# Kernel tuning notes

Measured on AMD Instinct MI355X. Metric: run time of the kernel, lower is better.

The kernel has to match this reference:

```python
import jax, jax.numpy as jnp
import numpy as np

N_NODES = 50000


def _gin_layer(feat, src, dst, W, b):
    # sum-aggregate neighbor (src) features onto dst nodes, eps=0
    agg = jax.ops.segment_sum(feat[src], dst, num_segments=N_NODES)
    return (feat + agg) @ W + b


def setup_inputs() -> dict:
    key = jax.random.key(0)
    ks = jax.random.split(key, 8)
    n, e, d, c = N_NODES, 1600000, 128, 4
    feat = jax.random.normal(ks[0], (n, d), dtype=jnp.float32)
    src = jax.random.randint(ks[1], (e,), 0, n, dtype=jnp.int64)
    dst = jax.random.randint(ks[2], (e,), 0, n, dtype=jnp.int64)
    s = 1.0 / np.sqrt(d)
    W0 = jax.random.normal(ks[3], (d, d), dtype=jnp.float32) * s
    W1 = jax.random.normal(ks[4], (d, d), dtype=jnp.float32) * s
    W2 = jax.random.normal(ks[5], (d, d), dtype=jnp.float32) * s
    W3 = jax.random.normal(ks[6], (d, c), dtype=jnp.float32) * s
    return {
        "feat": feat, "src": src, "dst": dst,
        "W0": W0, "b0": jnp.zeros((d,), jnp.float32),
        "W1": W1, "b1": jnp.zeros((d,), jnp.float32),
        "W2": W2, "b2": jnp.zeros((d,), jnp.float32),
        "W3": W3, "b3": jnp.zeros((c,), jnp.float32),
    }


def reference(feat, src, dst, W0, b0, W1, b1, W2, b2, W3, b3):
    # 3 hidden GINConv layers with ReLU (dropout p=0 / eval -> identity)
    h = jax.nn.relu(_gin_layer(feat, src, dst, W0, b0))
    h = jax.nn.relu(_gin_layer(h, src, dst, W1, b1))
    h = jax.nn.relu(_gin_layer(h, src, dst, W2, b2))
    # final GINConv, no activation
    return _gin_layer(h, src, dst, W3, b3)
```

## Files before the change

### kernel.cpp

```cpp
#include <hip/hip_runtime.h>
#include <hip/hip_bf16.h>

#define N_NODES 50000
#define NSLICE 8
#define SLICE_SZ 6250

__device__ __forceinline__ unsigned short f2bf(float f) {
    unsigned int u = __float_as_uint(f);
    unsigned int r = (u + 0x7fffu + ((u >> 16) & 1u)) >> 16;
    return (unsigned short)r;
}

__global__ void k_hist(const int* __restrict__ dst, int* __restrict__ deg, int ne) {
    int e = blockIdx.x * 256 + threadIdx.x;
    if (e < ne) {
        int d = __builtin_nontemporal_load(dst + e);
        atomicAdd(&deg[d], 1);
    }
}

__global__ __launch_bounds__(1024) void k_blocksum(const int* __restrict__ deg,
                                                   int* __restrict__ bsum) {
    int i = blockIdx.x * 1024 + threadIdx.x;
    int v = (i < N_NODES) ? deg[i] : 0;
#pragma unroll
    for (int off = 32; off >= 1; off >>= 1) v += __shfl_down(v, off, 64);
    __shared__ int ws[16];
    if ((threadIdx.x & 63) == 0) ws[threadIdx.x >> 6] = v;
    __syncthreads();
    if (threadIdx.x < 16) {
        int s = ws[threadIdx.x];
#pragma unroll
        for (int off = 8; off >= 1; off >>= 1) s += __shfl_down(s, off, 16);
        if (threadIdx.x == 0) bsum[blockIdx.x] = s;
    }
}

__global__ __launch_bounds__(1024) void k_scan2(const int* __restrict__ deg,
                                                const int* __restrict__ bsum,
                                                int* __restrict__ rowptr,
                                                int* __restrict__ cursor) {
    __shared__ int lds[1024];
    int b = blockIdx.x, t = threadIdx.x;
    int prefix = 0;
    for (int k = 0; k < b; ++k) prefix += bsum[k];
    int i = b * 1024 + t;
    int v = (i < N_NODES) ? deg[i] : 0;
    lds[t] = v;
    __syncthreads();
    for (int off = 1; off < 1024; off <<= 1) {
        int x = (t >= off) ? lds[t - off] : 0;
        __syncthreads();
        lds[t] += x;
        __syncthreads();
    }
    int excl = prefix + lds[t] - v;
    if (i <= N_NODES) {
        rowptr[i] = excl;
        if (i < N_NODES) cursor[i] = excl;
    }
}

__global__ __launch_bounds__(256) void k_fill(const int* __restrict__ src,
                                              const int* __restrict__ dst,
                                              int* __restrict__ cursor,
                                              unsigned short* __restrict__ col,
                                              int ne, int chunk) {
    int slice = blockIdx.x & (NSLICE - 1);
    int grp   = blockIdx.x >> 3;
    int lo = slice * SLICE_SZ;
    int hi = lo + SLICE_SZ;
    int start = grp * chunk;
    int end = start + chunk;
    if (end > ne) end = ne;
    for (int e = start + threadIdx.x; e < end; e += 256) {
        int d = __builtin_nontemporal_load(dst + e);
        int s = __builtin_nontemporal_load(src + e);
        if (d >= lo && d < hi) {
            int p = atomicAdd(&cursor[d], 1);
            col[p] = (unsigned short)s;
        }
    }
}

#define FMA4(a_, s_, v_) \
    do { (a_).x += (s_) * (v_).x; (a_).y += (s_) * (v_).y; \
         (a_).z += (s_) * (v_).z; (a_).w += (s_) * (v_).w; } while (0)

__global__ __launch_bounds__(256) void k_gemm128(const float* __restrict__ X,
                                                 const float* __restrict__ W,
                                                 unsigned short* __restrict__ G,
                                                 int nrows) {
    __shared__ float Ws[128 * 128];
    __shared__ float Xs[32 * 128];
    int t = threadIdx.x;
    int rowbase = blockIdx.x * 32;

    const float4* W4 = (const float4*)W;
    float4* Ws4 = (float4*)Ws;
#pragma unroll
    for (int i = 0; i < 16; ++i) Ws4[t + i * 256] = W4[t + i * 256];

    const float4* X4 = (const float4*)X;
    float4* Xs4 = (float4*)Xs;
#pragma unroll
    for (int i = 0; i < 4; ++i) {
        int idx = t + i * 256;
        int r = rowbase + (idx >> 5);
        Xs4[idx] = (r < nrows) ? X4[r * 32 + (idx & 31)] : make_float4(0.f, 0.f, 0.f, 0.f);
    }
    __syncthreads();

    int cg = t & 31;
    int rg = t >> 5;
    float4 acc[4];
#pragma unroll
    for (int r = 0; r < 4; ++r) acc[r] = make_float4(0.f, 0.f, 0.f, 0.f);

    for (int kk = 0; kk < 32; ++kk) {
        float4 x0 = Xs4[(rg * 4 + 0) * 32 + kk];
        float4 x1 = Xs4[(rg * 4 + 1) * 32 + kk];
        float4 x2 = Xs4[(rg * 4 + 2) * 32 + kk];
        float4 x3 = Xs4[(rg * 4 + 3) * 32 + kk];
        float4 w0 = Ws4[(kk * 4 + 0) * 32 + cg];
        float4 w1 = Ws4[(kk * 4 + 1) * 32 + cg];
        float4 w2 = Ws4[(kk * 4 + 2) * 32 + cg];
        float4 w3 = Ws4[(kk * 4 + 3) * 32 + cg];
        FMA4(acc[0], x0.x, w0); FMA4(acc[0], x0.y, w1); FMA4(acc[0], x0.z, w2); FMA4(acc[0], x0.w, w3);
        FMA4(acc[1], x1.x, w0); FMA4(acc[1], x1.y, w1); FMA4(acc[1], x1.z, w2); FMA4(acc[1], x1.w, w3);
        FMA4(acc[2], x2.x, w0); FMA4(acc[2], x2.y, w1); FMA4(acc[2], x2.z, w2); FMA4(acc[2], x2.w, w3);
        FMA4(acc[3], x3.x, w0); FMA4(acc[3], x3.y, w1); FMA4(acc[3], x3.z, w2); FMA4(acc[3], x3.w, w3);
    }

#pragma unroll
    for (int r = 0; r < 4; ++r) {
        int row = rowbase + rg * 4 + r;
        if (row < nrows) {
            ushort4 o;
            o.x = f2bf(acc[r].x); o.y = f2bf(acc[r].y);
            o.z = f2bf(acc[r].z); o.w = f2bf(acc[r].w);
            *(ushort4*)(G + (size_t)row * 128 + cg * 4) = o;
        }
    }
}

__global__ __launch_bounds__(256) void k_gather128(const unsigned short* __restrict__ g,
                                                   const int* __restrict__ rowptr,
                                                   const unsigned short* __restrict__ col,
                                                   const float* __restrict__ bias,
                                                   float* __restrict__ out,
                                                   int do_relu) {
    int node = blockIdx.x * 4 + (threadIdx.x >> 6);
    if (node >= N_NODES) return;
    int lane = threadIdx.x & 63;
    const unsigned int* g2 = (const unsigned int*)g;

    float2 bb = ((const float2*)bias)[lane];
    unsigned int sv = g2[(size_t)node * 64 + lane];
    float2 a0 = make_float2(bb.x + __uint_as_float(sv << 16),
                            bb.y + __uint_as_float(sv & 0xffff0000u));
    float2 a1 = make_float2(0.f, 0.f);
    float2 a2 = make_float2(0.f, 0.f);
    float2 a3 = make_float2(0.f, 0.f);

    int s = rowptr[node], e = rowptr[node + 1];
    int j = s;
    for (; j + 3 < e; j += 4) {
        int u0 = col[j], u1 = col[j + 1], u2 = col[j + 2], u3 = col[j + 3];
        unsigned int v0 = g2[(size_t)u0 * 64 + lane];
        unsigned int v1 = g2[(size_t)u1 * 64 + lane];
        unsigned int v2 = g2[(size_t)u2 * 64 + lane];
        unsigned int v3 = g2[(size_t)u3 * 64 + lane];
        a0.x += __uint_as_float(v0 << 16); a0.y += __uint_as_float(v0 & 0xffff0000u);
        a1.x += __uint_as_float(v1 << 16); a1.y += __uint_as_float(v1 & 0xffff0000u);
        a2.x += __uint_as_float(v2 << 16); a2.y += __uint_as_float(v2 & 0xffff0000u);
        a3.x += __uint_as_float(v3 << 16); a3.y += __uint_as_float(v3 & 0xffff0000u);
    }
    for (; j < e; ++j) {
        int u = col[j];
        unsigned int v = g2[(size_t)u * 64 + lane];
        a0.x += __uint_as_float(v << 16); a0.y += __uint_as_float(v & 0xffff0000u);
    }
    float2 acc = make_float2(a0.x + a1.x + a2.x + a3.x, a0.y + a1.y + a2.y + a3.y);
    if (do_relu) { acc.x = fmaxf(acc.x, 0.f); acc.y = fmaxf(acc.y, 0.f); }
    ((float2*)out)[(size_t)node * 64 + lane] = acc;
}

__global__ __launch_bounds__(256) void k_gemm_final(const float* __restrict__ X,
                                                    const float* __restrict__ W3,
                                                    float* __restrict__ Y, int nrows) {
    __shared__ float Ws[128 * 4];
    int t = threadIdx.x;
    if (t < 128) ((float4*)Ws)[t] = ((const float4*)W3)[t];
    __syncthreads();

    int idx = blockIdx.x * 256 + t;
    int row = idx >> 2;
    int q = idx & 3;
    if (row >= nrows) return;

    const float4* X4 = (const float4*)X;
    float acc[4] = {0.f, 0.f, 0.f, 0.f};
#pragma unroll
    for (int i = 0; i < 8; ++i) {
        float4 x = X4[row * 32 + q * 8 + i];
        int k = q * 32 + i * 4;
#pragma unroll
        for (int c = 0; c < 4; ++c) {
            acc[c] += x.x * Ws[(k + 0) * 4 + c] + x.y * Ws[(k + 1) * 4 + c]
                    + x.z * Ws[(k + 2) * 4 + c] + x.w * Ws[(k + 3) * 4 + c];
        }
    }
#pragma unroll
    for (int off = 1; off < 4; off <<= 1) {
#pragma unroll
        for (int c = 0; c < 4; ++c) acc[c] += __shfl_xor(acc[c], off, 64);
    }
    if (q == 0) ((float4*)Y)[row] = make_float4(acc[0], acc[1], acc[2], acc[3]);
}

__global__ __launch_bounds__(256) void k_gather4(const float* __restrict__ y,
                                                 const int* __restrict__ rowptr,
                                                 const unsigned short* __restrict__ col,
                                                 const float* __restrict__ b3,
                                                 float* __restrict__ out) {
    int v = blockIdx.x * 256 + threadIdx.x;
    if (v >= N_NODES) return;
    const float4* y4 = (const float4*)y;
    float4 acc = y4[v];
    float4 bb = *(const float4*)b3;
    acc.x += bb.x; acc.y += bb.y; acc.z += bb.z; acc.w += bb.w;
    int s = rowptr[v], e = rowptr[v + 1];
    for (int j = s; j < e; ++j) {
        float4 t = y4[col[j]];
        acc.x += t.x; acc.y += t.y; acc.z += t.z; acc.w += t.w;
    }
    ((float4*)out)[v] = acc;
}

extern "C" void kernel_launch(void* const* d_in, const int* in_sizes, int n_in,
                              void* d_out, int out_size, void* d_ws, size_t ws_size,
                              hipStream_t stream) {
    const float* feat = (const float*)d_in[0];
    const int*   src  = (const int*)d_in[1];
    const int*   dst  = (const int*)d_in[2];
    const float* W0 = (const float*)d_in[3];
    const float* b0 = (const float*)d_in[4];
    const float* W1 = (const float*)d_in[5];
    const float* b1 = (const float*)d_in[6];
    const float* W2 = (const float*)d_in[7];
    const float* b2 = (const float*)d_in[8];
    const float* W3 = (const float*)d_in[9];
    const float* b3 = (const float*)d_in[10];

    const int n  = N_NODES;
    const int ne = in_sizes[1];

    char* p = (char*)d_ws;
    auto alloc = [&](size_t bytes) {
        char* r = p;
        p += (bytes + 255) & ~(size_t)255;
        return r;
    };
    int*   rowptr = (int*)alloc((n + 1) * sizeof(int));
    int*   deg    = (int*)alloc(n * sizeof(int));
    int*   cursor = (int*)alloc(n * sizeof(int));
    int*   bsum   = (int*)alloc(64 * sizeof(int));
    unsigned short* col = (unsigned short*)alloc(ne * sizeof(unsigned short));
    unsigned short* g = (unsigned short*)alloc((size_t)n * 128 * sizeof(unsigned short));
    float* hA     = (float*)alloc((size_t)n * 128 * sizeof(float));
    float* hB     = (float*)alloc((size_t)n * 128 * sizeof(float));
    float* y      = (float*)alloc((size_t)n * 4 * sizeof(float));
    float* outf   = (float*)d_out;

    int eb = (ne + 255) / 256;
    int gemmb = (n + 31) / 32;
    int gathb = (n + 3) / 4;
    int nb256 = (n + 255) / 256;
    int scanb = (n + 1023) / 1024;

    const int BPS = 128;
    int chunk = (ne + BPS - 1) / BPS;

    hipMemsetAsync(deg, 0, n * sizeof(int), stream);
    k_hist<<<eb, 256, 0, stream>>>(dst, deg, ne);
    k_blocksum<<<scanb, 1024, 0, stream>>>(deg, bsum);
    k_scan2<<<scanb, 1024, 0, stream>>>(deg, bsum, rowptr, cursor);
    k_fill<<<NSLICE * BPS, 256, 0, stream>>>(src, dst, cursor, col, ne, chunk);

    k_gemm128<<<gemmb, 256, 0, stream>>>(feat, W0, g, n);
    k_gather128<<<gathb, 256, 0, stream>>>(g, rowptr, col, b0, hA, 1);
    k_gemm128<<<gemmb, 256, 0, stream>>>(hA, W1, g, n);
    k_gather128<<<gathb, 256, 0, stream>>>(g, rowptr, col, b1, hB, 1);
    k_gemm128<<<gemmb, 256, 0, stream>>>(hB, W2, g, n);
    k_gather128<<<gathb, 256, 0, stream>>>(g, rowptr, col, b2, hA, 1);
    k_gemm_final<<<(n * 4 + 255) / 256, 256, 0, stream>>>(hA, W3, y, n);
    k_gather4<<<nb256, 256, 0, stream>>>(y, rowptr, col, b3, outf);
}
```

Measured before the change: 533.1 us.

## Vectorize edge loads in hist/fill and split gather across half-wavefronts

Measured after the change: 514.6 us. -3.5%, faster.

```diff
diff --git a/kernel.cpp b/kernel.cpp
--- a/kernel.cpp
+++ b/kernel.cpp
@@ -4,6 +4,8 @@
 #define N_NODES 50000
 #define NSLICE 8
 #define SLICE_SZ 6250
+
+typedef int int4v __attribute__((ext_vector_type(4)));
 
 __device__ __forceinline__ unsigned short f2bf(float f) {
     unsigned int u = __float_as_uint(f);
@@ -12,10 +14,16 @@
 }
 
 __global__ void k_hist(const int* __restrict__ dst, int* __restrict__ deg, int ne) {
-    int e = blockIdx.x * 256 + threadIdx.x;
-    if (e < ne) {
-        int d = __builtin_nontemporal_load(dst + e);
-        atomicAdd(&deg[d], 1);
+    int g = blockIdx.x * 256 + threadIdx.x;
+    int e = g * 4;
+    if (e + 3 < ne) {
+        int4v d = __builtin_nontemporal_load((const int4v*)(dst + e));
+        atomicAdd(&deg[d.x], 1);
+        atomicAdd(&deg[d.y], 1);
+        atomicAdd(&deg[d.z], 1);
+        atomicAdd(&deg[d.w], 1);
+    } else if (e < ne) {
+        for (int k = 0; k < 4 && e + k < ne; ++k) atomicAdd(&deg[dst[e + k]], 1);
     }
 }
 
@@ -65,20 +73,38 @@
                                               const int* __restrict__ dst,
                                               int* __restrict__ cursor,
                                               unsigned short* __restrict__ col,
-                                              int ne, int chunk) {
+                                              int ne, int ng4, int chunk4) {
     int slice = blockIdx.x & (NSLICE - 1);
     int grp   = blockIdx.x >> 3;
     int lo = slice * SLICE_SZ;
     int hi = lo + SLICE_SZ;
-    int start = grp * chunk;
-    int end = start + chunk;
-    if (end > ne) end = ne;
-    for (int e = start + threadIdx.x; e < end; e += 256) {
-        int d = __builtin_nontemporal_load(dst + e);
-        int s = __builtin_nontemporal_load(src + e);
-        if (d >= lo && d < hi) {
-            int p = atomicAdd(&cursor[d], 1);
-            col[p] = (unsigned short)s;
+    int g0 = grp * chunk4;
+    int g1 = g0 + chunk4;
+    if (g1 > ng4) g1 = ng4;
+    for (int g = g0 + threadIdx.x; g < g1; g += 256) {
+        int e = g * 4;
+        if (e + 3 < ne) {
+            int4v d = __builtin_nontemporal_load((const int4v*)(dst + e));
+            bool m0 = (d.x >= lo) && (d.x < hi);
+            bool m1 = (d.y >= lo) && (d.y < hi);
+            bool m2 = (d.z >= lo) && (d.z < hi);
+            bool m3 = (d.w >= lo) && (d.w < hi);
+            if (m0 | m1 | m2 | m3) {
+                int4v s = __builtin_nontemporal_load((const int4v*)(src + e));
+                if (m0) { int p = atomicAdd(&cursor[d.x], 1); col[p] = (unsigned short)s.x; }
+                if (m1) { int p = atomicAdd(&cursor[d.y], 1); col[p] = (unsigned short)s.y; }
+                if (m2) { int p = atomicAdd(&cursor[d.z], 1); col[p] = (unsigned short)s.z; }
+                if (m3) { int p = atomicAdd(&cursor[d.w], 1); col[p] = (unsigned short)s.w; }
+            }
+        } else {
+            for (int k = 0; k < 4 && e + k < ne; ++k) {
+                int dd = dst[e + k];
+                if (dd >= lo && dd < hi) {
+                    int ss = src[e + k];
+                    int p = atomicAdd(&cursor[dd], 1);
+                    col[p] = (unsigned short)ss;
+                }
+            }
         }
     }
 }
@@ -144,6 +170,12 @@
     }
 }
 
+#define ACC4(a_, v_) \
+    do { (a_).x += __uint_as_float((v_).x << 16); \
+         (a_).y += __uint_as_float((v_).x & 0xffff0000u); \
+         (a_).z += __uint_as_float((v_).y << 16); \
+         (a_).w += __uint_as_float((v_).y & 0xffff0000u); } while (0)
+
 __global__ __launch_bounds__(256) void k_gather128(const unsigned short* __restrict__ g,
                                                    const int* __restrict__ rowptr,
                                                    const unsigned short* __restrict__ col,
@@ -153,37 +185,52 @@
     int node = blockIdx.x * 4 + (threadIdx.x >> 6);
     if (node >= N_NODES) return;
     int lane = threadIdx.x & 63;
-    const unsigned int* g2 = (const unsigned int*)g;
-
-    float2 bb = ((const float2*)bias)[lane];
-    unsigned int sv = g2[(size_t)node * 64 + lane];
-    float2 a0 = make_float2(bb.x + __uint_as_float(sv << 16),
-                            bb.y + __uint_as_float(sv & 0xffff0000u));
-    float2 a1 = make_float2(0.f, 0.f);
-    float2 a2 = make_float2(0.f, 0.f);
-    float2 a3 = make_float2(0.f, 0.f);
+    int li = lane & 31;
+    int half = lane >> 5;
+    const uint2* g2 = (const uint2*)g;
+
+    float4 a0 = make_float4(0.f, 0.f, 0.f, 0.f);
+    float4 a1 = make_float4(0.f, 0.f, 0.f, 0.f);
+    float4 a2 = make_float4(0.f, 0.f, 0.f, 0.f);
+    float4 a3 = make_float4(0.f, 0.f, 0.f, 0.f);
 
     int s = rowptr[node], e = rowptr[node + 1];
-    int j = s;
-    for (; j + 3 < e; j += 4) {
-        int u0 = col[j], u1 = col[j + 1], u2 = col[j + 2], u3 = col[j + 3];
-        unsigned int v0 = g2[(size_t)u0 * 64 + lane];
-        unsigned int v1 = g2[(size_t)u1 * 64 + lane];
-        unsigned int v2 = g2[(size_t)u2 * 64 + lane];
-        unsigned int v3 = g2[(size_t)u3 * 64 + lane];
-        a0.x += __uint_as_float(v0 << 16); a0.y += __uint_as_float(v0 & 0xffff0000u);
-        a1.x += __uint_as_float(v1 << 16); a1.y += __uint_as_float(v1 & 0xffff0000u);
-        a2.x += __uint_as_float(v2 << 16); a2.y += __uint_as_float(v2 & 0xffff0000u);
-        a3.x += __uint_as_float(v3 << 16); a3.y += __uint_as_float(v3 & 0xffff0000u);
-    }
-    for (; j < e; ++j) {
+    int j = s + half;
+    for (; j + 6 < e; j += 8) {
+        int u0 = col[j], u1 = col[j + 2], u2 = col[j + 4], u3 = col[j + 6];
+        uint2 v0 = g2[(size_t)u0 * 32 + li];
+        uint2 v1 = g2[(size_t)u1 * 32 + li];
+        uint2 v2 = g2[(size_t)u2 * 32 + li];
+        uint2 v3 = g2[(size_t)u3 * 32 + li];
+        ACC4(a0, v0); ACC4(a1, v1); ACC4(a2, v2); ACC4(a3, v3);
+    }
+    for (; j < e; j += 2) {
         int u = col[j];
-        unsigned int v = g2[(size_t)u * 64 + lane];
-        a0.x += __uint_as_float(v << 16); a0.y += __uint_as_float(v & 0xffff0000u);
-    }
-    float2 acc = make_float2(a0.x + a1.x + a2.x + a3.x, a0.y + a1.y + a2.y + a3.y);
-    if (do_relu) { acc.x = fmaxf(acc.x, 0.f); acc.y = fmaxf(acc.y, 0.f); }
-    ((float2*)out)[(size_t)node * 64 + lane] = acc;
+        uint2 v = g2[(size_t)u * 32 + li];
+        ACC4(a0, v);
+    }
+    float4 acc = make_float4(a0.x + a1.x + a2.x + a3.x,
+                             a0.y + a1.y + a2.y + a3.y,
+                             a0.z + a1.z + a2.z + a3.z,
+                             a0.w + a1.w + a2.w + a3.w);
+    acc.x += __shfl_xor(acc.x, 32, 64);
+    acc.y += __shfl_xor(acc.y, 32, 64);
+    acc.z += __shfl_xor(acc.z, 32, 64);
+    acc.w += __shfl_xor(acc.w, 32, 64);
+
+    if (half == 0) {
+        uint2 sv = g2[(size_t)node * 32 + li];
+        float4 bb = ((const float4*)bias)[li];
+        acc.x += bb.x + __uint_as_float(sv.x << 16);
+        acc.y += bb.y + __uint_as_float(sv.x & 0xffff0000u);
+        acc.z += bb.z + __uint_as_float(sv.y << 16);
+        acc.w += bb.w + __uint_as_float(sv.y & 0xffff0000u);
+        if (do_relu) {
+            acc.x = fmaxf(acc.x, 0.f); acc.y = fmaxf(acc.y, 0.f);
+            acc.z = fmaxf(acc.z, 0.f); acc.w = fmaxf(acc.w, 0.f);
+        }
+        ((float4*)out)[(size_t)node * 32 + li] = acc;
+    }
 }
 
 __global__ __launch_bounds__(256) void k_gemm_final(const float* __restrict__ X,
@@ -273,20 +320,22 @@
     float* y      = (float*)alloc((size_t)n * 4 * sizeof(float));
     float* outf   = (float*)d_out;
 
-    int eb = (ne + 255) / 256;
     int gemmb = (n + 31) / 32;
     int gathb = (n + 3) / 4;
     int nb256 = (n + 255) / 256;
     int scanb = (n + 1023) / 1024;
 
+    int ng4 = (ne + 3) / 4;
+    int histb = (ng4 + 255) / 256;
+
     const int BPS = 128;
-    int chunk = (ne + BPS - 1) / BPS;
+    int chunk4 = (ng4 + BPS - 1) / BPS;
 
     hipMemsetAsync(deg, 0, n * sizeof(int), stream);
-    k_hist<<<eb, 256, 0, stream>>>(dst, deg, ne);
+    k_hist<<<histb, 256, 0, stream>>>(dst, deg, ne);
     k_blocksum<<<scanb, 1024, 0, stream>>>(deg, bsum);
     k_scan2<<<scanb, 1024, 0, stream>>>(deg, bsum, rowptr, cursor);
-    k_fill<<<NSLICE * BPS, 256, 0, stream>>>(src, dst, cursor, col, ne, chunk);
+    k_fill<<<NSLICE * BPS, 256, 0, stream>>>(src, dst, cursor, col, ne, ng4, chunk4);
 
     k_gemm128<<<gemmb, 256, 0, stream>>>(feat, W0, g, n);
     k_gather128<<<gathb, 256, 0, stream>>>(g, rowptr, col, b0, hA, 1);
```
